# Kernel tuning notes

Hardware: AMD Instinct MI355X
Metric: run time of the kernel (lower is better)

## Reference

```python
import jax, jax.numpy as jnp
import numpy as np

N_NODES = 100000
N_EDGES = 1600000
MSG_DIM = 16
HID_DIM = 16
N_ETYPE = 16
N_CLASSES = 64


def setup_inputs() -> dict:
    key = jax.random.key(0)
    ks = jax.random.split(key, 11)
    s = 1.0 / np.sqrt(HID_DIM)
    return {
        "features": jax.random.normal(ks[0], (N_NODES, HID_DIM), dtype=jnp.float32),
        "src": jax.random.randint(ks[1], (N_EDGES,), 0, N_NODES, dtype=jnp.int32),
        "dst": jax.random.randint(ks[2], (N_EDGES,), 0, N_NODES, dtype=jnp.int32),
        "e_type": jax.random.randint(ks[3], (N_EDGES,), 0, N_ETYPE, dtype=jnp.int32),
        "edge_emb": jax.random.normal(ks[4], (N_ETYPE, MSG_DIM * HID_DIM), dtype=jnp.float32),
        "W_ih": jax.random.uniform(ks[5], (3 * HID_DIM, MSG_DIM), dtype=jnp.float32, minval=-s, maxval=s),
        "W_hh": jax.random.uniform(ks[6], (3 * HID_DIM, HID_DIM), dtype=jnp.float32, minval=-s, maxval=s),
        "b_ih": jax.random.uniform(ks[7], (3 * HID_DIM,), dtype=jnp.float32, minval=-s, maxval=s),
        "b_hh": jax.random.uniform(ks[8], (3 * HID_DIM,), dtype=jnp.float32, minval=-s, maxval=s),
        "W_out": jax.random.normal(ks[9], (N_CLASSES, HID_DIM), dtype=jnp.float32) * s,
        "b_out": jax.random.normal(ks[10], (N_CLASSES,), dtype=jnp.float32) * 0.01,
    }


def reference(features, src, dst, e_type, edge_emb, W_ih, W_hh, b_ih, b_hh, W_out, b_out):
    # Per-edge message: A_e @ h_src, A_e = edge-type embedding reshaped [msg, hid]
    A = edge_emb[e_type].reshape(-1, MSG_DIM, HID_DIM)          # [E, M, H]
    msg = jnp.einsum("emh,eh->em", A, features[src])            # [E, M]
    # Sum-aggregate messages into destination nodes
    m = jax.ops.segment_sum(msg, dst, num_segments=N_NODES)     # [N, M]
    # Single-step GRU (PyTorch gate order: r, z, n)
    gx = m @ W_ih.T + b_ih                                      # [N, 3H]
    gh = features @ W_hh.T + b_hh                               # [N, 3H]
    xr, xz, xn = jnp.split(gx, 3, axis=-1)
    hr, hz, hn = jnp.split(gh, 3, axis=-1)
    r = jax.nn.sigmoid(xr + hr)
    z = jax.nn.sigmoid(xz + hz)
    n = jnp.tanh(xn + r * hn)
    h = (1.0 - z) * n + z * features                            # [N, H]
    return h @ W_out.T + b_out                                  # [N, C]
```

## Files before the change

### kernel.cpp

```cpp
#include <hip/hip_runtime.h>

#define NNODES 100000
#define NEDGES 1600000
#define HID 16
#define MSG 16
#define NTYPE 16
#define NCLS 64

#define BSH 7
#define NBK ((NNODES + 127) >> 7)
#define CHSZ 8192
#define NCH ((NEDGES + CHSZ - 1) / CHSZ)
#define BCAP 2304
#define BLKPB 5
#define AGG_BLOCKS (NBK * BLKPB)

#define ASTR 20
#define ATY  320

#define MAGG_N (NNODES * MSG)

__device__ __forceinline__ float sigmoid_f(float x) {
    return 1.0f / (1.0f + __expf(-x));
}
__device__ __forceinline__ float tanh_f(float x) {
    x = fminf(fmaxf(x, -15.0f), 15.0f);
    float e = __expf(2.0f * x);
    return (e - 1.0f) / (e + 1.0f);
}

__global__ __launch_bounds__(1024) void scat_k(const int* __restrict__ src,
                                               const int* __restrict__ dst,
                                               const int* __restrict__ et,
                                               int* __restrict__ gcnt,
                                               int* __restrict__ rec,
                                               float* __restrict__ magg) {
    __shared__ int cnt[NBK];
    const int t = threadIdx.x, ch = blockIdx.x;

    {
        const int per = (MAGG_N / 4 + NCH - 1) / NCH;
        float4* m4 = (float4*)magg;
        int s0 = ch * per;
        int s1 = s0 + per; if (s1 > MAGG_N / 4) s1 = MAGG_N / 4;
        const float4 z = {0.f, 0.f, 0.f, 0.f};
        for (int k = s0 + t; k < s1; k += 1024) m4[k] = z;
    }

    for (int k = t; k < NBK; k += 1024) cnt[k] = 0;
    __syncthreads();
    int dcache[CHSZ / 1024];
    #pragma unroll
    for (int k = 0; k < CHSZ / 1024; k++) {
        int e = ch * CHSZ + k * 1024 + t;
        dcache[k] = (e < NEDGES) ? dst[e] : -1;
        if (dcache[k] >= 0) atomicAdd(&cnt[dcache[k] >> BSH], 1);
    }
    __syncthreads();
    for (int k = t; k < NBK; k += 1024) {
        int c = cnt[k];
        cnt[k] = c ? atomicAdd(&gcnt[k], c) : 0;
    }
    __syncthreads();
    #pragma unroll
    for (int k = 0; k < CHSZ / 1024; k++) {
        int e = ch * CHSZ + k * 1024 + t;
        if (e < NEDGES) {
            int d = dcache[k];
            int b = d >> BSH;
            int pos = atomicAdd(&cnt[b], 1);
            rec[b * BCAP + pos] = src[e] | (et[e] << 17) | ((d & 127) << 21);
        }
    }
}

__global__ __launch_bounds__(512) void sort2_k(const int* __restrict__ gcnt,
                                               int* __restrict__ rec) {
    __shared__ int buf[BCAP];
    __shared__ int cnt[128];
    __shared__ int basec[128];
    __shared__ int wtot[4];
    const int t = threadIdx.x, b = blockIdx.x;
    const int jb = b * BCAP;
    const int len = gcnt[b];
    if (len <= 0) return;

    if (t < 128) cnt[t] = 0;
    for (int k = t; k < len; k += 512) buf[k] = rec[jb + k];
    __syncthreads();
    for (int k = t; k < len; k += 512) atomicAdd(&cnt[((unsigned)buf[k]) >> 21], 1);
    __syncthreads();
    int v = (t < 128) ? cnt[t] : 0;
    int lane = t & 63, w = t >> 6;
    int s = v;
    #pragma unroll
    for (int d = 1; d < 64; d <<= 1) {
        int u = __shfl_up(s, d, 64);
        if (lane >= d) s += u;
    }
    if (lane == 63 && w < 2) wtot[w] = s;
    __syncthreads();
    if (t < 128) basec[t] = s - v + (w == 1 ? wtot[0] : 0);
    __syncthreads();
    for (int k = t; k < len; k += 512) {
        int r = buf[k];
        int p = atomicAdd(&basec[((unsigned)r) >> 21], 1);
        rec[jb + p] = r;
    }
}

__global__ __launch_bounds__(512) void agg3_k(const float* __restrict__ feat,
                                              const int* __restrict__ rec,
                                              const int* __restrict__ gcnt,
                                              const float* __restrict__ edge_emb,
                                              float* __restrict__ magg) {
    __shared__ float At2[NTYPE * ATY];
    __shared__ int recs[512];
    const int t = threadIdx.x;
    const int b  = blockIdx.x / BLKPB;
    const int br = blockIdx.x % BLKPB;
    const int cnt = gcnt[b];
    const int w0 = br << 9;
    if (w0 >= cnt) return;

    #pragma unroll
    for (int idx = t; idx < NTYPE * MSG * HID; idx += 512) {
        int ty = idx >> 8, rem = idx & 255, ii = rem >> 4, h = rem & 15;
        At2[ty * ATY + ii * ASTR + h] = edge_emb[idx];
    }
    {
        int ns = BCAP - w0; ns = ns > 512 ? 512 : ns;
        if (t < ns) recs[t] = rec[b * BCAP + w0 + t];
    }
    __syncthreads();

    const int g = t >> 4, i = t & 15;
    const int base = g << 4;
    int vr = cnt - (w0 + base);
    if (vr <= 0) return;
    const int vcnt = vr > 16 ? 16 : vr;

    float macc = 0.0f;
    int cur = -1;
    #pragma unroll 1
    for (int p = 0; p < 16; p += 2) {
        if (p >= vcnt) break;
        const bool has2 = (p + 1) < vcnt;
        int r1 = recs[base + p];
        int r2 = has2 ? recs[base + p + 1] : r1;
        const float4* f1 = (const float4*)(feat + (size_t)(r1 & 0x1FFFF) * HID);
        const float4* f2 = (const float4*)(feat + (size_t)(r2 & 0x1FFFF) * HID);
        float4 Fa0 = f1[0], Fa1 = f1[1], Fa2 = f1[2], Fa3 = f1[3];
        float4 Fb0 = f2[0], Fb1 = f2[1], Fb2 = f2[2], Fb3 = f2[3];
        __builtin_amdgcn_sched_barrier(0);

        {
            const float4* pa = (const float4*)(At2 + ((r1 >> 17) & 15) * ATY + i * ASTR);
            float4 A0 = pa[0], A1 = pa[1], A2 = pa[2], A3 = pa[3];
            float m1;
            m1  = A0.x*Fa0.x + A0.y*Fa0.y + A0.z*Fa0.z + A0.w*Fa0.w;
            m1 += A1.x*Fa1.x + A1.y*Fa1.y + A1.z*Fa1.z + A1.w*Fa1.w;
            m1 += A2.x*Fa2.x + A2.y*Fa2.y + A2.z*Fa2.z + A2.w*Fa2.w;
            m1 += A3.x*Fa3.x + A3.y*Fa3.y + A3.z*Fa3.z + A3.w*Fa3.w;
            int d1 = (b << BSH) | (((unsigned)r1) >> 21);
            if (d1 != cur) {
                if (cur >= 0) atomicAdd(&magg[(size_t)cur * MSG + i], macc);
                macc = 0.0f; cur = d1;
            }
            macc += m1;
        }
        if (has2) {
            const float4* pb = (const float4*)(At2 + ((r2 >> 17) & 15) * ATY + i * ASTR);
            float4 B0 = pb[0], B1 = pb[1], B2 = pb[2], B3 = pb[3];
            float m2;
            m2  = B0.x*Fb0.x + B0.y*Fb0.y + B0.z*Fb0.z + B0.w*Fb0.w;
            m2 += B1.x*Fb1.x + B1.y*Fb1.y + B1.z*Fb1.z + B1.w*Fb1.w;
            m2 += B2.x*Fb2.x + B2.y*Fb2.y + B2.z*Fb2.z + B2.w*Fb2.w;
            m2 += B3.x*Fb3.x + B3.y*Fb3.y + B3.z*Fb3.z + B3.w*Fb3.w;
            int d2 = (b << BSH) | (((unsigned)r2) >> 21);
            if (d2 != cur) {
                atomicAdd(&magg[(size_t)cur * MSG + i], macc);
                macc = 0.0f; cur = d2;
            }
            macc += m2;
        }
    }
    atomicAdd(&magg[(size_t)cur * MSG + i], macc);
}

__global__ __launch_bounds__(256) void ggnn_edge(
    const float* __restrict__ feat,
    const int* __restrict__ src,
    const int* __restrict__ dst,
    const int* __restrict__ etype,
    const float* __restrict__ edge_emb,
    float* __restrict__ magg)
{
    __shared__ float At[NTYPE * MSG * HID];
    for (int idx = threadIdx.x; idx < NTYPE * MSG * HID; idx += 256) {
        int ty = idx >> 8, rem = idx & 255, i = rem >> 4, hh = rem & 15;
        At[(ty << 8) | (hh << 4) | i] = edge_emb[idx];
    }
    __syncthreads();
    const long long total = (long long)NEDGES * MSG;
    for (long long w = (long long)blockIdx.x * 256 + threadIdx.x; w < total;
         w += (long long)gridDim.x * 256) {
        const int e = (int)(w >> 4);
        const int i = (int)(w & 15);
        const int s = src[e];
        const int d = dst[e];
        const int ty = etype[e];
        const float4* fp = (const float4*)(feat + (size_t)s * HID);
        const float4 f0 = fp[0], f1 = fp[1], f2 = fp[2], f3 = fp[3];
        const float* a = At + (ty << 8) + i;
        float m;
        m  = a[0*16]*f0.x + a[1*16]*f0.y + a[2*16]*f0.z + a[3*16]*f0.w;
        m += a[4*16]*f1.x + a[5*16]*f1.y + a[6*16]*f1.z + a[7*16]*f1.w;
        m += a[8*16]*f2.x + a[9*16]*f2.y + a[10*16]*f2.z + a[11*16]*f2.w;
        m += a[12*16]*f3.x + a[13*16]*f3.y + a[14*16]*f3.z + a[15*16]*f3.w;
        atomicAdd(magg + (size_t)d * MSG + i, m);
    }
}

__global__ __launch_bounds__(256) void node_k(
    const float* __restrict__ feat,
    const float* __restrict__ magg,
    const float* __restrict__ W_ih,
    const float* __restrict__ W_hh,
    const float* __restrict__ b_ih,
    const float* __restrict__ b_hh,
    const float* __restrict__ W_out,
    const float* __restrict__ b_out,
    float* __restrict__ out)
{
    __shared__ float hn_s[256 * 20];
    const int t = threadIdx.x;
    const int n = blockIdx.x * 256 + t;
    if (n < NNODES) {
        float hv[HID], mv[MSG];
        const float4* hp = (const float4*)(feat + (size_t)n * HID);
        const float4* mp = (const float4*)(magg + (size_t)n * MSG);
        #pragma unroll
        for (int q = 0; q < 4; q++) {
            float4 a = hp[q];
            hv[4*q+0] = a.x; hv[4*q+1] = a.y; hv[4*q+2] = a.z; hv[4*q+3] = a.w;
            float4 c = mp[q];
            mv[4*q+0] = c.x; mv[4*q+1] = c.y; mv[4*q+2] = c.z; mv[4*q+3] = c.w;
        }
        #pragma unroll
        for (int i = 0; i < HID; i++) {
            float xr = b_ih[i], xz = b_ih[16 + i], xn = b_ih[32 + i];
            float hr = b_hh[i], hz = b_hh[16 + i], hn = b_hh[32 + i];
            #pragma unroll
            for (int j = 0; j < HID; j++) {
                xr += W_ih[(i)      * 16 + j] * mv[j];
                xz += W_ih[(16 + i) * 16 + j] * mv[j];
                xn += W_ih[(32 + i) * 16 + j] * mv[j];
                hr += W_hh[(i)      * 16 + j] * hv[j];
                hz += W_hh[(16 + i) * 16 + j] * hv[j];
                hn += W_hh[(32 + i) * 16 + j] * hv[j];
            }
            float r  = sigmoid_f(xr + hr);
            float z  = sigmoid_f(xz + hz);
            float nn = tanh_f(xn + r * hn);
            hn_s[t * 20 + i] = (1.0f - z) * nn + z * hv[i];
        }
    }
    __syncthreads();

    const int w = t >> 6, g = (t >> 4) & 3, li = t & 15;
    float4 w4[4][4];
    #pragma unroll
    for (int rr = 0; rr < 4; rr++)
        #pragma unroll
        for (int qq = 0; qq < 4; qq++)
            w4[rr][qq] = ((const float4*)W_out)[(4 * li + rr) * 4 + qq];
    const float4 bo4 = ((const float4*)b_out)[li];
    const int nb = blockIdx.x * 256;

    #pragma unroll
    for (int it = 0; it < 16; it++) {
        int ln = it * 16 + w * 4 + g;
        int n2 = nb + ln;
        if (n2 < NNODES) {
            const float4* hq = (const float4*)(hn_s + ln * 20);
            float4 h0 = hq[0], h1 = hq[1], h2 = hq[2], h3 = hq[3];
            float4 o;
            o.x = bo4.x + w4[0][0].x*h0.x + w4[0][0].y*h0.y + w4[0][0].z*h0.z + w4[0][0].w*h0.w
                        + w4[0][1].x*h1.x + w4[0][1].y*h1.y + w4[0][1].z*h1.z + w4[0][1].w*h1.w
                        + w4[0][2].x*h2.x + w4[0][2].y*h2.y + w4[0][2].z*h2.z + w4[0][2].w*h2.w
                        + w4[0][3].x*h3.x + w4[0][3].y*h3.y + w4[0][3].z*h3.z + w4[0][3].w*h3.w;
            o.y = bo4.y + w4[1][0].x*h0.x + w4[1][0].y*h0.y + w4[1][0].z*h0.z + w4[1][0].w*h0.w
                        + w4[1][1].x*h1.x + w4[1][1].y*h1.y + w4[1][1].z*h1.z + w4[1][1].w*h1.w
                        + w4[1][2].x*h2.x + w4[1][2].y*h2.y + w4[1][2].z*h2.z + w4[1][2].w*h2.w
                        + w4[1][3].x*h3.x + w4[1][3].y*h3.y + w4[1][3].z*h3.z + w4[1][3].w*h3.w;
            o.z = bo4.z + w4[2][0].x*h0.x + w4[2][0].y*h0.y + w4[2][0].z*h0.z + w4[2][0].w*h0.w
                        + w4[2][1].x*h1.x + w4[2][1].y*h1.y + w4[2][1].z*h1.z + w4[2][1].w*h1.w
                        + w4[2][2].x*h2.x + w4[2][2].y*h2.y + w4[2][2].z*h2.z + w4[2][2].w*h2.w
                        + w4[2][3].x*h3.x + w4[2][3].y*h3.y + w4[2][3].z*h3.z + w4[2][3].w*h3.w;
            o.w = bo4.w + w4[3][0].x*h0.x + w4[3][0].y*h0.y + w4[3][0].z*h0.z + w4[3][0].w*h0.w
                        + w4[3][1].x*h1.x + w4[3][1].y*h1.y + w4[3][1].z*h1.z + w4[3][1].w*h1.w
                        + w4[3][2].x*h2.x + w4[3][2].y*h2.y + w4[3][2].z*h2.z + w4[3][2].w*h2.w
                        + w4[3][3].x*h3.x + w4[3][3].y*h3.y + w4[3][3].z*h3.z + w4[3][3].w*h3.w;
            ((float4*)(out + (size_t)n2 * NCLS))[li] = o;
        }
    }
}

extern "C" void kernel_launch(void* const* d_in, const int* in_sizes, int n_in,
                              void* d_out, int out_size, void* d_ws, size_t ws_size,
                              hipStream_t stream) {
    const float* feat     = (const float*)d_in[0];
    const int*   src      = (const int*)d_in[1];
    const int*   dst      = (const int*)d_in[2];
    const int*   etype    = (const int*)d_in[3];
    const float* edge_emb = (const float*)d_in[4];
    const float* W_ih     = (const float*)d_in[5];
    const float* W_hh     = (const float*)d_in[6];
    const float* b_ih     = (const float*)d_in[7];
    const float* b_hh     = (const float*)d_in[8];
    const float* W_out    = (const float*)d_in[9];
    const float* b_out    = (const float*)d_in[10];
    float* out = (float*)d_out;

    float* magg = (float*)d_ws;
    int*   gcnt = (int*)d_ws + (size_t)MAGG_N;
    int*   rec  = gcnt + 1024;
    size_t need = ((size_t)MAGG_N + 1024 + (size_t)NBK * BCAP) * 4;

    if (ws_size >= need) {
        hipMemsetAsync(gcnt, 0, 1024 * sizeof(int), stream);
        scat_k  <<<NCH, 1024, 0, stream>>>(src, dst, etype, gcnt, rec, magg);
        sort2_k <<<NBK, 512, 0, stream>>>(gcnt, rec);
        agg3_k  <<<AGG_BLOCKS, 512, 0, stream>>>(feat, rec, gcnt, edge_emb, magg);
    } else {
        hipMemsetAsync(magg, 0, (size_t)MAGG_N * sizeof(float), stream);
        ggnn_edge<<<2560, 256, 0, stream>>>(feat, src, dst, etype, edge_emb, magg);
    }
    node_k<<<(NNODES + 255) / 256, 256, 0, stream>>>(
        feat, magg, W_ih, W_hh, b_ih, b_hh, W_out, b_out, out);
}
```

Baseline: 134.3 us.

## Sort bucket records by edge type and accumulate messages in shared memory

The per-bucket sort now orders records by edge type instead of destination node, so groups of threads read the same A matrix from shared memory. The aggregation kernel no longer relies on destination-sorted runs. It accumulates messages into a per-block shared-memory tile with LDS atomics and flushes non-zero entries to global memory with one atomic each. This trades run-length merging for LDS atomics, which may contend, plus a fixed flush of 2048 entries per block. The sort also gets cheaper: a 16-entry count instead of a 128-entry scan.

Measured after the change: 229.0 us. +70.6%, slower.

```diff
diff --git a/kernel.cpp b/kernel.cpp
--- a/kernel.cpp
+++ b/kernel.cpp
@@ -74,47 +74,41 @@
     }
 }
 
-__global__ __launch_bounds__(512) void sort2_k(const int* __restrict__ gcnt,
+__global__ __launch_bounds__(512) void sortt_k(const int* __restrict__ gcnt,
                                                int* __restrict__ rec) {
     __shared__ int buf[BCAP];
-    __shared__ int cnt[128];
-    __shared__ int basec[128];
-    __shared__ int wtot[4];
+    __shared__ int cnt16[NTYPE];
+    __shared__ int base16[NTYPE];
     const int t = threadIdx.x, b = blockIdx.x;
     const int jb = b * BCAP;
     const int len = gcnt[b];
-    if (len <= 0) return;
-
-    if (t < 128) cnt[t] = 0;
+    if (len <= 0 || len > BCAP) return;
+
+    if (t < NTYPE) cnt16[t] = 0;
     for (int k = t; k < len; k += 512) buf[k] = rec[jb + k];
     __syncthreads();
-    for (int k = t; k < len; k += 512) atomicAdd(&cnt[((unsigned)buf[k]) >> 21], 1);
-    __syncthreads();
-    int v = (t < 128) ? cnt[t] : 0;
-    int lane = t & 63, w = t >> 6;
-    int s = v;
-    #pragma unroll
-    for (int d = 1; d < 64; d <<= 1) {
-        int u = __shfl_up(s, d, 64);
-        if (lane >= d) s += u;
-    }
-    if (lane == 63 && w < 2) wtot[w] = s;
-    __syncthreads();
-    if (t < 128) basec[t] = s - v + (w == 1 ? wtot[0] : 0);
+    for (int k = t; k < len; k += 512) atomicAdd(&cnt16[(buf[k] >> 17) & 15], 1);
+    __syncthreads();
+    if (t == 0) {
+        int run = 0;
+        #pragma unroll
+        for (int q = 0; q < NTYPE; q++) { base16[q] = run; run += cnt16[q]; }
+    }
     __syncthreads();
     for (int k = t; k < len; k += 512) {
         int r = buf[k];
-        int p = atomicAdd(&basec[((unsigned)r) >> 21], 1);
+        int p = atomicAdd(&base16[(r >> 17) & 15], 1);
         rec[jb + p] = r;
     }
 }
 
-__global__ __launch_bounds__(512) void agg3_k(const float* __restrict__ feat,
+__global__ __launch_bounds__(512) void agg5_k(const float* __restrict__ feat,
                                               const int* __restrict__ rec,
                                               const int* __restrict__ gcnt,
                                               const float* __restrict__ edge_emb,
                                               float* __restrict__ magg) {
     __shared__ float At2[NTYPE * ATY];
+    __shared__ float acc[128 * 17];
     __shared__ int recs[512];
     const int t = threadIdx.x;
     const int b  = blockIdx.x / BLKPB;
@@ -128,6 +122,7 @@
         int ty = idx >> 8, rem = idx & 255, ii = rem >> 4, h = rem & 15;
         At2[ty * ATY + ii * ASTR + h] = edge_emb[idx];
     }
+    for (int k = t; k < 128 * 17; k += 512) acc[k] = 0.0f;
     {
         int ns = BCAP - w0; ns = ns > 512 ? 512 : ns;
         if (t < ns) recs[t] = rec[b * BCAP + w0 + t];
@@ -137,11 +132,8 @@
     const int g = t >> 4, i = t & 15;
     const int base = g << 4;
     int vr = cnt - (w0 + base);
-    if (vr <= 0) return;
-    const int vcnt = vr > 16 ? 16 : vr;
-
-    float macc = 0.0f;
-    int cur = -1;
+    const int vcnt = vr < 0 ? 0 : (vr > 16 ? 16 : vr);
+
     #pragma unroll 1
     for (int p = 0; p < 16; p += 2) {
         if (p >= vcnt) break;
@@ -162,12 +154,7 @@
             m1 += A1.x*Fa1.x + A1.y*Fa1.y + A1.z*Fa1.z + A1.w*Fa1.w;
             m1 += A2.x*Fa2.x + A2.y*Fa2.y + A2.z*Fa2.z + A2.w*Fa2.w;
             m1 += A3.x*Fa3.x + A3.y*Fa3.y + A3.z*Fa3.z + A3.w*Fa3.w;
-            int d1 = (b << BSH) | (((unsigned)r1) >> 21);
-            if (d1 != cur) {
-                if (cur >= 0) atomicAdd(&magg[(size_t)cur * MSG + i], macc);
-                macc = 0.0f; cur = d1;
-            }
-            macc += m1;
+            atomicAdd(&acc[(((unsigned)r1) >> 21) * 17 + i], m1);
         }
         if (has2) {
             const float4* pb = (const float4*)(At2 + ((r2 >> 17) & 15) * ATY + i * ASTR);
@@ -177,15 +164,18 @@
             m2 += B1.x*Fb1.x + B1.y*Fb1.y + B1.z*Fb1.z + B1.w*Fb1.w;
             m2 += B2.x*Fb2.x + B2.y*Fb2.y + B2.z*Fb2.z + B2.w*Fb2.w;
             m2 += B3.x*Fb3.x + B3.y*Fb3.y + B3.z*Fb3.z + B3.w*Fb3.w;
-            int d2 = (b << BSH) | (((unsigned)r2) >> 21);
-            if (d2 != cur) {
-                atomicAdd(&magg[(size_t)cur * MSG + i], macc);
-                macc = 0.0f; cur = d2;
-            }
-            macc += m2;
-        }
-    }
-    atomicAdd(&magg[(size_t)cur * MSG + i], macc);
+            atomicAdd(&acc[(((unsigned)r2) >> 21) * 17 + i], m2);
+        }
+    }
+    __syncthreads();
+
+    const int nb = b << BSH;
+    for (int k = t; k < 128 * 16; k += 512) {
+        int ln = k >> 4, ii = k & 15;
+        int n = nb + ln;
+        float v = acc[ln * 17 + ii];
+        if (n < NNODES && v != 0.0f) atomicAdd(&magg[(size_t)n * MSG + ii], v);
+    }
 }
 
 __global__ __launch_bounds__(256) void ggnn_edge(
@@ -331,8 +321,8 @@
     if (ws_size >= need) {
         hipMemsetAsync(gcnt, 0, 1024 * sizeof(int), stream);
         scat_k  <<<NCH, 1024, 0, stream>>>(src, dst, etype, gcnt, rec, magg);
-        sort2_k <<<NBK, 512, 0, stream>>>(gcnt, rec);
-        agg3_k  <<<AGG_BLOCKS, 512, 0, stream>>>(feat, rec, gcnt, edge_emb, magg);
+        sortt_k <<<NBK, 512, 0, stream>>>(gcnt, rec);
+        agg5_k  <<<AGG_BLOCKS, 512, 0, stream>>>(feat, rec, gcnt, edge_emb, magg);
     } else {
         hipMemsetAsync(magg, 0, (size_t)MAGG_N * sizeof(float), stream);
         ggnn_edge<<<2560, 256, 0, stream>>>(feat, src, dst, etype, edge_emb, magg);
```
